# Optimization experiments

Hardware: AMD Instinct MI355X
Metric: run time of the kernel (lower is better)

## Reference

```python
import jax, jax.numpy as jnp
import numpy as np

NB_CLS, NB_QRY, NB_SHOT, FEAT_DIM = 5, 75, 5, 640
Q_STEPS, LR_DNI, HID = 3, 1e-3, 4096
N = NB_CLS + NB_QRY           # nodes in similarity graph (80)
M = 1 + N                     # subgraph size (81)
# strict upper triangle of MxM minus the query-query block (matches triu_index_input)
_t = np.ones((M, M)); _t[1 + NB_CLS:, 1 + NB_CLS:] = 0
_t = np.triu(_t, 1)
MASK_IDX = jnp.asarray(np.flatnonzero(_t.ravel() == 1))
DNI_IN = int(MASK_IDX.shape[0])  # 465


def _pairwise(supp, query):
    feat = jnp.concatenate([supp, query], 0)
    nrm = jnp.maximum(jnp.linalg.norm(feat, axis=-1, keepdims=True), 1e-12)
    feat = feat / nrm
    sim = feat @ feat.T                      # (N, N)
    sim_ss = sim[:NB_CLS, :NB_CLS]
    sim_qq = sim[NB_CLS:, NB_CLS:]
    sim_sq = sim[:NB_CLS, NB_CLS:]
    sim_feat_support = jnp.concatenate([sim_ss, sim_sq], 1).T   # (N, nb_cls)
    sim_feat_query = jnp.concatenate([sim_sq, sim_qq], 0)       # (N, nb_qry)
    return sim_feat_support, sim_feat_query, sim_sq


def _subgraph(sim_s, sim_q):
    # topk indices are constants wrt grad (no_grad in torch; ints in jax)
    idx_q = jax.lax.top_k(sim_q, NB_QRY)[1] + NB_CLS
    idx_s = jax.lax.top_k(sim_s, NB_CLS)[1]
    index = jnp.concatenate([jnp.arange(N, dtype=idx_s.dtype)[:, None], idx_s, idx_q], 1)  # (N, M)
    sim = jnp.concatenate([sim_s, sim_q], 1)                     # (N, N)
    sub = sim[index[:, :, None], index[:, None, :]]              # (N, M, M) batched gather
    return sub.reshape(N, M * M)[:, MASK_IDX]                    # (N, DNI_IN)


def _dni(x, W1, b1, W2, b2, W3, b3):
    h = jax.nn.relu(x @ W1.T + b1)
    h = jax.nn.relu(h @ W2.T + b2)
    return h @ W3.T + b3


def _refine(supp, query, ds, dq):
    for _ in range(Q_STEPS):
        inputs, vjp = jax.vjp(lambda s: _subgraph(*_pairwise(s, query)[:2]), supp)
        supp = supp - LR_DNI * vjp(_dni(inputs, *ds))[0]
        inputs, vjp = jax.vjp(lambda q: _subgraph(*_pairwise(supp, q)[:2]), query)
        query = query - LR_DNI * vjp(_dni(inputs, *dq))[0]
    return supp, query


def setup_inputs() -> dict:
    key = jax.random.key(0)
    ks = jax.random.split(key, 16)
    d = {
        "feat_support": jax.random.normal(ks[0], (NB_CLS, NB_SHOT, FEAT_DIM), jnp.float32),
        "feat_query": jax.random.normal(ks[1], (NB_QRY, FEAT_DIM), jnp.float32),
        "scale_cls": jnp.full((1,), 10.0, jnp.float32),
    }
    names = ["ds_W1", "ds_b1", "ds_W2", "ds_b2", "ds_W3", "ds_b3",
             "dq_W1", "dq_b1", "dq_W2", "dq_b2", "dq_W3", "dq_b3"]
    shapes = [(HID, DNI_IN), (HID,), (HID, HID), (HID,), (DNI_IN, HID), (DNI_IN,)] * 2
    for i, (n, sh) in enumerate(zip(names, shapes)):
        d[n] = jax.random.normal(ks[2 + i], sh, jnp.float32) * 0.02
    return d


def reference(feat_support, feat_query, scale_cls,
              ds_W1, ds_b1, ds_W2, ds_b2, ds_W3, ds_b3,
              dq_W1, dq_b1, dq_W2, dq_b2, dq_W3, dq_b3):
    supp = feat_support.mean(1)                                  # (nb_cls, feat_dim)
    ds = (ds_W1, ds_b1, ds_W2, ds_b2, ds_W3, ds_b3)
    dq = (dq_W1, dq_b1, dq_W2, dq_b2, dq_W3, dq_b3)
    supp, query = _refine(supp, feat_query, ds, dq)
    _, _, sim_sq = _pairwise(supp, query)
    return (sim_sq * scale_cls).T                                # (nb_qry, nb_cls)
```

## Files before the change

### kernel.cpp

```cpp
#include <hip/hip_runtime.h>

#define NCLS 5
#define NQRY 75
#define NTOT 80
#define FD   640
#define HIDN 4096
#define DNIN 465
#define KPAD 512
#define NPAD 512
#define LRDNI 1e-3f

#define KS1 8
#define KS2 16
#define KS3 32

typedef short  v8s __attribute__((ext_vector_type(8)));
typedef float  v4f __attribute__((ext_vector_type(4)));

__device__ __forceinline__ ushort f2bf(float x) {
    uint u = __float_as_uint(x);
    u = (u + 0x7FFFu + ((u >> 16) & 1u)) >> 16;
    return (ushort)u;
}
__device__ __forceinline__ uint pk2(float a, float b) {
    return (uint)f2bf(a) | ((uint)f2bf(b) << 16);
}

__global__ void k_init(const float* __restrict__ fs, const float* __restrict__ fq,
                       float* __restrict__ supp, float* __restrict__ qbuf) {
    int idx = blockIdx.x * 256 + threadIdx.x;
    if (idx < NCLS * FD) {
        int c = idx / FD, d = idx % FD;
        float s = 0.f;
        #pragma unroll
        for (int t = 0; t < 5; t++) s += fs[(c * 5 + t) * FD + d];
        supp[idx] = s * 0.2f;
    }
    if (idx < NQRY * FD) qbuf[idx] = fq[idx];
}

__global__ void k_cvtW1(const float* __restrict__ W, ushort* __restrict__ Wb) {
    int idx = blockIdx.x * 256 + threadIdx.x;
    int r = idx >> 9, c = idx & 511;
    Wb[idx] = (c < DNIN) ? f2bf(W[r * DNIN + c]) : (ushort)0;
}
__global__ void k_cvtW3(const float* __restrict__ W, ushort* __restrict__ Wb) {
    int idx = blockIdx.x * 256 + threadIdx.x;
    int r = idx >> 12;
    Wb[idx] = (r < DNIN) ? f2bf(W[idx]) : (ushort)0;
}
__global__ void k_cvtW2(const float* __restrict__ W, ushort* __restrict__ Wb) {
    int idx = blockIdx.x * 256 + threadIdx.x;
    float4 v = ((const float4*)W)[idx];
    uint2 q; q.x = pk2(v.x, v.y); q.y = pk2(v.z, v.w);
    ((uint2*)Wb)[idx] = q;
}

__device__ __forceinline__ const float* rowptr(const float* supp, const float* qbuf, int r) {
    return (r < NCLS) ? (supp + r * FD) : (qbuf + (r - NCLS) * FD);
}

template<bool FIN>
__global__ void k_simrank(const float* __restrict__ supp, const float* __restrict__ qbuf,
                          float* __restrict__ f, float* __restrict__ nrm,
                          float* __restrict__ S, int* __restrict__ perm,
                          const float* __restrict__ scale, float* __restrict__ out) {
    __shared__ float fi[FD];
    __shared__ float row[NTOT];
    __shared__ float ssh[NTOT];
    int i = blockIdx.x;
    int t = threadIdx.x;
    const float* ri = rowptr(supp, qbuf, i);
    for (int u = t; u < FD; u += 128) fi[u] = ri[u];
    __syncthreads();
    float dot = 0.f;
    if (t < NTOT) {
        const float* rj = rowptr(supp, qbuf, t);
        float ss = 0.f;
        for (int k = 0; k < FD; k += 4) {
            float4 a = *(const float4*)(fi + k);
            float4 b = *(const float4*)(rj + k);
            dot += a.x * b.x + a.y * b.y + a.z * b.z + a.w * b.w;
            ss  += b.x * b.x + b.y * b.y + b.z * b.z + b.w * b.w;
        }
        ssh[t] = ss;
    }
    __syncthreads();
    float ni = fmaxf(sqrtf(ssh[i]), 1e-12f);
    float inv_i = 1.0f / ni;
    if (t < NTOT) {
        float nt = fmaxf(sqrtf(ssh[t]), 1e-12f);
        float val = dot * inv_i / nt;
        if (FIN) {
            if (t >= NCLS) out[(t - NCLS) * NCLS + i] = val * scale[0];
        } else {
            row[t] = val;
            S[i * NTOT + t] = val;
        }
    }
    if (FIN) return;
    __syncthreads();
    for (int u = t; u < FD; u += 128) f[i * FD + u] = fi[u] * inv_i;
    if (t == 0) { nrm[i] = ni; perm[i * 81] = i; }
    if (t < NCLS) {
        float v = row[t]; int rank = 0;
        for (int k = 0; k < NCLS; k++) {
            float w = row[k];
            if (w > v || (w == v && k < t)) rank++;
        }
        perm[i * 81 + 1 + rank] = t;
    } else if (t < NTOT) {
        int j = t - NCLS; float v = row[t]; int rank = 0;
        for (int k = NCLS; k < NTOT; k++) {
            float w = row[k];
            if (w > v || (w == v && (k - NCLS) < j)) rank++;
        }
        perm[i * 81 + 6 + rank] = t;
    }
}

__device__ __forceinline__ void mask_ab(int m, int& a, int& b) {
    int start = 0, len = 80, aa = 0;
    while (m >= start + len) { start += len; len--; aa++; }
    a = aa; b = aa + 1 + (m - start);
}

__global__ void k_gather(const float* __restrict__ S, const int* __restrict__ perm,
                         ushort* __restrict__ Xb, float* __restrict__ Gs) {
    __shared__ int p[81];
    int i = blockIdx.x;
    int t = threadIdx.x;
    if (t < 81) p[t] = perm[i * 81 + t];
    if (t < NTOT) Gs[i * NTOT + t] = 0.f;
    __syncthreads();
    if (t < DNIN) {
        int a, b; mask_ab(t, a, b);
        Xb[i * KPAD + t] = f2bf(S[p[a] * NTOT + p[b]]);
    } else if (t < KPAD) {
        Xb[i * KPAD + t] = 0;
    }
}

template<int NT, int KSTEPS>
__global__ __launch_bounds__(256) void k_gemm(
        const ushort* __restrict__ A, int lda,
        const ushort* __restrict__ B, int ldb,
        float* __restrict__ C, int ldc) {
    int tid = threadIdx.x;
    int w = tid >> 6, lane = tid & 63, l16 = lane & 15, quad = lane >> 4;
    int n0 = blockIdx.x * (NT * 64) + w * NT * 16;
    int kc0 = blockIdx.y * (KSTEPS * 32);
    const ushort* Ap = A + l16 * lda + kc0 + quad * 8;
    const ushort* Bp = B + (size_t)(n0 + l16) * ldb + kc0 + quad * 8;

    v4f acc[5][NT];
    #pragma unroll
    for (int mt = 0; mt < 5; mt++)
        #pragma unroll
        for (int nt = 0; nt < NT; nt++) acc[mt][nt] = (v4f){0.f, 0.f, 0.f, 0.f};

    #pragma unroll
    for (int s = 0; s < KSTEPS; s++) {
        int ko = s * 32;
        v8s a[5], b[NT];
        #pragma unroll
        for (int mt = 0; mt < 5; mt++)
            a[mt] = *(const v8s*)(Ap + mt * 16 * lda + ko);
        #pragma unroll
        for (int nt = 0; nt < NT; nt++)
            b[nt] = *(const v8s*)(Bp + nt * 16 * ldb + ko);
        #pragma unroll
        for (int mt = 0; mt < 5; mt++)
            #pragma unroll
            for (int nt = 0; nt < NT; nt++)
                acc[mt][nt] = __builtin_amdgcn_mfma_f32_16x16x32_bf16(a[mt], b[nt], acc[mt][nt], 0, 0, 0);
    }
    float* Cp = C + (size_t)blockIdx.y * 80 * ldc;
    #pragma unroll
    for (int nt = 0; nt < NT; nt++) {
        int col = n0 + nt * 16 + l16;
        #pragma unroll
        for (int mt = 0; mt < 5; mt++)
            #pragma unroll
            for (int r = 0; r < 4; r++)
                Cp[(mt * 16 + quad * 4 + r) * ldc + col] = acc[mt][nt][r];
    }
}

template<int NS>
__global__ void k_ep(const float* __restrict__ P, const float* __restrict__ bias,
                     ushort* __restrict__ H) {
    int idx = blockIdx.x * 256 + threadIdx.x;
    float4 s = ((const float4*)bias)[idx & 1023];
    #pragma unroll
    for (int ks = 0; ks < NS; ks++) {
        float4 p = ((const float4*)P)[ks * (80 * HIDN / 4) + idx];
        s.x += p.x; s.y += p.y; s.z += p.z; s.w += p.w;
    }
    uint2 q;
    q.x = pk2(fmaxf(s.x, 0.f), fmaxf(s.y, 0.f));
    q.y = pk2(fmaxf(s.z, 0.f), fmaxf(s.w, 0.f));
    ((uint2*)H)[idx] = q;
}

__global__ void k_scatter(const float* __restrict__ P3, const float* __restrict__ b3,
                          const int* __restrict__ perm, float* __restrict__ Gs) {
    __shared__ int p[81];
    int i = blockIdx.x;
    int t = threadIdx.x;
    if (t < 81) p[t] = perm[i * 81 + t];
    __syncthreads();
    if (t < DNIN) {
        float g = b3[t];
        #pragma unroll
        for (int ks = 0; ks < KS3; ks++) g += P3[ks * (80 * NPAD) + i * NPAD + t];
        int a, b; mask_ab(t, a, b);
        atomicAdd(&Gs[p[a] * NTOT + p[b]], g);
    }
}

__global__ void k_bwd(const float* __restrict__ Gs, const float* __restrict__ f,
                      const float* __restrict__ nrm, float* __restrict__ target,
                      int row0) {
    int r = row0 + blockIdx.x;
    __shared__ float cj[NTOT];
    __shared__ float red[2];
    int t = threadIdx.x;
    if (t < NTOT) cj[t] = Gs[r * NTOT + t] + Gs[t * NTOT + r];
    __syncthreads();
    float df[5] = {0.f, 0.f, 0.f, 0.f, 0.f};
    for (int j = 0; j < NTOT; j++) {
        float c = cj[j];
        const float* fj = f + j * FD;
        #pragma unroll
        for (int u = 0; u < 5; u++) df[u] += c * fj[t + 128 * u];
    }
    const float* fr = f + r * FD;
    float frv[5]; float partial = 0.f;
    #pragma unroll
    for (int u = 0; u < 5; u++) { frv[u] = fr[t + 128 * u]; partial += df[u] * frv[u]; }
    #pragma unroll
    for (int o = 32; o > 0; o >>= 1) partial += __shfl_xor(partial, o, 64);
    if ((t & 63) == 0) red[t >> 6] = partial;
    __syncthreads();
    float dot = red[0] + red[1];
    float invn = 1.0f / nrm[r];
    float* dst = target + blockIdx.x * FD;
    #pragma unroll
    for (int u = 0; u < 5; u++) {
        float dx = (df[u] - dot * frv[u]) * invn;
        dst[t + 128 * u] -= LRDNI * dx;
    }
}

extern "C" void kernel_launch(void* const* d_in, const int* in_sizes, int n_in,
                              void* d_out, int out_size, void* d_ws, size_t ws_size,
                              hipStream_t stream) {
    const float* fs    = (const float*)d_in[0];
    const float* fq    = (const float*)d_in[1];
    const float* scale = (const float*)d_in[2];
    const float* W[12];
    for (int i = 0; i < 12; i++) W[i] = (const float*)d_in[3 + i];

    float* base = (float*)d_ws;
    float* supp = base;
    float* qbuf = supp + 3200;
    float* f    = qbuf + 48000;
    float* nrm  = f + 51200;
    float* S    = nrm + 96;
    int*   perm = (int*)(S + 6400);
    float* P1   = (float*)(perm + 6496);
    float* P2   = P1 + (size_t)KS1 * 80 * HIDN;
    float* P3   = P2 + (size_t)KS2 * 80 * HIDN;
    float* Gs   = P3 + (size_t)KS3 * 80 * NPAD;
    ushort* Xb  = (ushort*)(Gs + 6400);
    ushort* H1b = Xb + 80 * KPAD;
    ushort* H2b = H1b + 80 * HIDN;
    ushort* W1b_ds = H2b + 80 * HIDN;
    ushort* W1b_dq = W1b_ds + HIDN * KPAD;
    ushort* W3b_ds = W1b_dq + HIDN * KPAD;
    ushort* W3b_dq = W3b_ds + NPAD * HIDN;
    ushort* W2b_ds = W3b_dq + NPAD * HIDN;
    ushort* W2b_dq = W2b_ds + (size_t)HIDN * HIDN;

    k_cvtW1<<<8192, 256, 0, stream>>>(W[0],  W1b_ds);
    k_cvtW1<<<8192, 256, 0, stream>>>(W[6],  W1b_dq);
    k_cvtW3<<<8192, 256, 0, stream>>>(W[4],  W3b_ds);
    k_cvtW3<<<8192, 256, 0, stream>>>(W[10], W3b_dq);
    k_cvtW2<<<16384, 256, 0, stream>>>(W[2], W2b_ds);
    k_cvtW2<<<16384, 256, 0, stream>>>(W[8], W2b_dq);
    k_init<<<188, 256, 0, stream>>>(fs, fq, supp, qbuf);

    for (int step = 0; step < 3; step++) {
        for (int half = 0; half < 2; half++) {
            const float* const* w = (half == 0) ? W : (W + 6);
            const ushort* W1b = (half == 0) ? W1b_ds : W1b_dq;
            const ushort* W2b = (half == 0) ? W2b_ds : W2b_dq;
            const ushort* W3b = (half == 0) ? W3b_ds : W3b_dq;
            k_simrank<false><<<80, 128, 0, stream>>>(supp, qbuf, f, nrm, S, perm, nullptr, nullptr);
            k_gather<<<80, 512, 0, stream>>>(S, perm, Xb, Gs);
            k_gemm<1, 2><<<dim3(64, KS1), 256, 0, stream>>>(Xb, KPAD, W1b, KPAD, P1, HIDN);
            k_ep<KS1><<<320, 256, 0, stream>>>(P1, w[1], H1b);
            k_gemm<2, 8><<<dim3(32, KS2), 256, 0, stream>>>(H1b, HIDN, W2b, HIDN, P2, HIDN);
            k_ep<KS2><<<320, 256, 0, stream>>>(P2, w[3], H2b);
            k_gemm<1, 4><<<dim3(8, KS3), 256, 0, stream>>>(H2b, HIDN, W3b, HIDN, P3, NPAD);
            k_scatter<<<80, 512, 0, stream>>>(P3, w[5], perm, Gs);
            if (half == 0) k_bwd<<<5, 128, 0, stream>>>(Gs, f, nrm, supp, 0);
            else           k_bwd<<<75, 128, 0, stream>>>(Gs, f, nrm, qbuf, NCLS);
        }
    }
    k_simrank<true><<<5, 128, 0, stream>>>(supp, qbuf, f, nrm, S, perm, scale, (float*)d_out);
}
```

Measured before the change: 659.0 us.

## Pre-swizzle weights into MFMA fragment layout and fuse setup kernels

Weight matrices are converted to bf16 in a tiled fragment-major layout, so each lane's B operand for a 16x32 MFMA tile sits contiguously and a wavefront reads 1 KB in one coalesced burst instead of strided rows. The six conversion kernels and the init kernel are merged into one grid-stride setup kernel to cut launch count. The first GEMM's K-split drops from 8 to 4 with more K steps per block, which reduces partial-sum traffic. The setup kernel's layout transform reads W1 with scattered scalar loads, which may cost more than before.

Result: faster. 633.0 us (-3.9%).

```diff
diff --git a/kernel.cpp b/kernel.cpp
--- a/kernel.cpp
+++ b/kernel.cpp
@@ -10,7 +10,7 @@
 #define NPAD 512
 #define LRDNI 1e-3f
 
-#define KS1 8
+#define KS1 4
 #define KS2 16
 #define KS3 32
 
@@ -26,34 +26,67 @@
     return (uint)f2bf(a) | ((uint)f2bf(b) << 16);
 }
 
-__global__ void k_init(const float* __restrict__ fs, const float* __restrict__ fq,
-                       float* __restrict__ supp, float* __restrict__ qbuf) {
-    int idx = blockIdx.x * 256 + threadIdx.x;
-    if (idx < NCLS * FD) {
-        int c = idx / FD, d = idx % FD;
+__global__ void k_setup(const float* __restrict__ fs, const float* __restrict__ fq,
+                        const float* __restrict__ W1s, const float* __restrict__ W1q,
+                        const float* __restrict__ W2s, const float* __restrict__ W2q,
+                        const float* __restrict__ W3s, const float* __restrict__ W3q,
+                        ushort* __restrict__ W1bs, ushort* __restrict__ W1bq,
+                        ushort* __restrict__ W2bs, ushort* __restrict__ W2bq,
+                        ushort* __restrict__ W3bs, ushort* __restrict__ W3bq,
+                        float* __restrict__ supp, float* __restrict__ qbuf) {
+    int stride = gridDim.x * 256;
+    int tid = blockIdx.x * 256 + threadIdx.x;
+    for (int o = tid; o < 524288; o += stride) {
+        int oo = o & 262143;
+        const float* Ws = (o < 262144) ? W1s : W1q;
+        ushort* Wd = (o < 262144) ? W1bs : W1bq;
+        int l = oo & 63, ks = (oo >> 6) & 15, nt = oo >> 10;
+        int n = nt * 16 + (l & 15), kb = ks * 32 + ((l >> 4) << 3);
+        ushort tmp[8];
+        #pragma unroll
+        for (int j = 0; j < 8; j++) {
+            int k = kb + j;
+            tmp[j] = (k < DNIN) ? f2bf(Ws[n * DNIN + k]) : (ushort)0;
+        }
+        *(uint4*)(Wd + (size_t)oo * 8) = *(uint4*)tmp;
+    }
+    for (int o = tid; o < 524288; o += stride) {
+        int oo = o & 262143;
+        const float* Ws = (o < 262144) ? W3s : W3q;
+        ushort* Wd = (o < 262144) ? W3bs : W3bq;
+        int l = oo & 63, ks = (oo >> 6) & 127, nt = oo >> 13;
+        int n = nt * 16 + (l & 15), kb = ks * 32 + ((l >> 4) << 3);
+        uint4 q;
+        if (n < DNIN) {
+            float4 f0 = *(const float4*)(Ws + (size_t)n * HIDN + kb);
+            float4 f1 = *(const float4*)(Ws + (size_t)n * HIDN + kb + 4);
+            q.x = pk2(f0.x, f0.y); q.y = pk2(f0.z, f0.w);
+            q.z = pk2(f1.x, f1.y); q.w = pk2(f1.z, f1.w);
+        } else q = (uint4){0, 0, 0, 0};
+        *(uint4*)(Wd + (size_t)oo * 8) = q;
+    }
+    for (int o = tid; o < 4194304; o += stride) {
+        int oo = o & 2097151;
+        const float* Ws = (o < 2097152) ? W2s : W2q;
+        ushort* Wd = (o < 2097152) ? W2bs : W2bq;
+        int l = oo & 63, ks = (oo >> 6) & 127, nt = oo >> 13;
+        int n = nt * 16 + (l & 15), kb = ks * 32 + ((l >> 4) << 3);
+        float4 f0 = *(const float4*)(Ws + (size_t)n * HIDN + kb);
+        float4 f1 = *(const float4*)(Ws + (size_t)n * HIDN + kb + 4);
+        uint4 q;
+        q.x = pk2(f0.x, f0.y); q.y = pk2(f0.z, f0.w);
+        q.z = pk2(f1.x, f1.y); q.w = pk2(f1.z, f1.w);
+        *(uint4*)(Wd + (size_t)oo * 8) = q;
+    }
+    for (int o = tid; o < NCLS * FD; o += stride) {
+        int c = o / FD, d = o % FD;
         float s = 0.f;
         #pragma unroll
         for (int t = 0; t < 5; t++) s += fs[(c * 5 + t) * FD + d];
-        supp[idx] = s * 0.2f;
-    }
-    if (idx < NQRY * FD) qbuf[idx] = fq[idx];
-}
-
-__global__ void k_cvtW1(const float* __restrict__ W, ushort* __restrict__ Wb) {
-    int idx = blockIdx.x * 256 + threadIdx.x;
-    int r = idx >> 9, c = idx & 511;
-    Wb[idx] = (c < DNIN) ? f2bf(W[r * DNIN + c]) : (ushort)0;
-}
-__global__ void k_cvtW3(const float* __restrict__ W, ushort* __restrict__ Wb) {
-    int idx = blockIdx.x * 256 + threadIdx.x;
-    int r = idx >> 12;
-    Wb[idx] = (r < DNIN) ? f2bf(W[idx]) : (ushort)0;
-}
-__global__ void k_cvtW2(const float* __restrict__ W, ushort* __restrict__ Wb) {
-    int idx = blockIdx.x * 256 + threadIdx.x;
-    float4 v = ((const float4*)W)[idx];
-    uint2 q; q.x = pk2(v.x, v.y); q.y = pk2(v.z, v.w);
-    ((uint2*)Wb)[idx] = q;
+        supp[o] = s * 0.2f;
+    }
+    for (int o = tid; o < NQRY * FD / 4; o += stride)
+        ((float4*)qbuf)[o] = ((const float4*)fq)[o];
 }
 
 __device__ __forceinline__ const float* rowptr(const float* supp, const float* qbuf, int r) {
@@ -144,14 +177,14 @@
 template<int NT, int KSTEPS>
 __global__ __launch_bounds__(256) void k_gemm(
         const ushort* __restrict__ A, int lda,
-        const ushort* __restrict__ B, int ldb,
+        const ushort* __restrict__ Bf, int nks,
         float* __restrict__ C, int ldc) {
     int tid = threadIdx.x;
     int w = tid >> 6, lane = tid & 63, l16 = lane & 15, quad = lane >> 4;
     int n0 = blockIdx.x * (NT * 64) + w * NT * 16;
     int kc0 = blockIdx.y * (KSTEPS * 32);
     const ushort* Ap = A + l16 * lda + kc0 + quad * 8;
-    const ushort* Bp = B + (size_t)(n0 + l16) * ldb + kc0 + quad * 8;
+    const ushort* Bp = Bf + ((size_t)(n0 >> 4) * nks + (kc0 >> 5)) * 512 + lane * 8;
 
     v4f acc[5][NT];
     #pragma unroll
@@ -161,14 +194,13 @@
 
     #pragma unroll
     for (int s = 0; s < KSTEPS; s++) {
-        int ko = s * 32;
         v8s a[5], b[NT];
         #pragma unroll
         for (int mt = 0; mt < 5; mt++)
-            a[mt] = *(const v8s*)(Ap + mt * 16 * lda + ko);
+            a[mt] = *(const v8s*)(Ap + mt * 16 * lda + s * 32);
         #pragma unroll
         for (int nt = 0; nt < NT; nt++)
-            b[nt] = *(const v8s*)(Bp + nt * 16 * ldb + ko);
+            b[nt] = *(const v8s*)(Bp + ((size_t)nt * nks + s) * 512);
         #pragma unroll
         for (int mt = 0; mt < 5; mt++)
             #pragma unroll
@@ -283,13 +315,9 @@
     ushort* W2b_ds = W3b_dq + NPAD * HIDN;
     ushort* W2b_dq = W2b_ds + (size_t)HIDN * HIDN;
 
-    k_cvtW1<<<8192, 256, 0, stream>>>(W[0],  W1b_ds);
-    k_cvtW1<<<8192, 256, 0, stream>>>(W[6],  W1b_dq);
-    k_cvtW3<<<8192, 256, 0, stream>>>(W[4],  W3b_ds);
-    k_cvtW3<<<8192, 256, 0, stream>>>(W[10], W3b_dq);
-    k_cvtW2<<<16384, 256, 0, stream>>>(W[2], W2b_ds);
-    k_cvtW2<<<16384, 256, 0, stream>>>(W[8], W2b_dq);
-    k_init<<<188, 256, 0, stream>>>(fs, fq, supp, qbuf);
+    k_setup<<<1024, 256, 0, stream>>>(fs, fq, W[0], W[6], W[2], W[8], W[4], W[10],
+                                      W1b_ds, W1b_dq, W2b_ds, W2b_dq, W3b_ds, W3b_dq,
+                                      supp, qbuf);
 
     for (int step = 0; step < 3; step++) {
         for (int half = 0; half < 2; half++) {
@@ -299,11 +327,11 @@
             const ushort* W3b = (half == 0) ? W3b_ds : W3b_dq;
             k_simrank<false><<<80, 128, 0, stream>>>(supp, qbuf, f, nrm, S, perm, nullptr, nullptr);
             k_gather<<<80, 512, 0, stream>>>(S, perm, Xb, Gs);
-            k_gemm<1, 2><<<dim3(64, KS1), 256, 0, stream>>>(Xb, KPAD, W1b, KPAD, P1, HIDN);
+            k_gemm<1, 4><<<dim3(64, KS1), 256, 0, stream>>>(Xb, KPAD, W1b, 16, P1, HIDN);
             k_ep<KS1><<<320, 256, 0, stream>>>(P1, w[1], H1b);
-            k_gemm<2, 8><<<dim3(32, KS2), 256, 0, stream>>>(H1b, HIDN, W2b, HIDN, P2, HIDN);
+            k_gemm<2, 8><<<dim3(32, KS2), 256, 0, stream>>>(H1b, HIDN, W2b, 128, P2, HIDN);
             k_ep<KS2><<<320, 256, 0, stream>>>(P2, w[3], H2b);
-            k_gemm<1, 4><<<dim3(8, KS3), 256, 0, stream>>>(H2b, HIDN, W3b, HIDN, P3, NPAD);
+            k_gemm<1, 4><<<dim3(8, KS3), 256, 0, stream>>>(H2b, HIDN, W3b, 128, P3, NPAD);
             k_scatter<<<80, 512, 0, stream>>>(P3, w[5], perm, Gs);
             if (half == 0) k_bwd<<<5, 128, 0, stream>>>(Gs, f, nrm, supp, 0);
             else           k_bwd<<<75, 128, 0, stream>>>(Gs, f, nrm, qbuf, NCLS);
```
